# Kernel tuning notes

Measured on AMD Instinct MI355X. Metric: run time of the kernel, lower is better.

The kernel has to match this reference:

```python
import jax, jax.numpy as jnp
import numpy as np

N_NODES = 100000
N_EDGES = 1600000
NEG_SLOPE = 0.2


def gat_conv(x, W, al, ar, src, dst, n_nodes):
    """DGL-style GATConv. x:[N,Fin] W:[Fin,H*D] al,ar:[H,D] -> [N,H,D]."""
    H, D = al.shape
    h = (x @ W).reshape(-1, H, D)                      # [N,H,D]
    el = jnp.sum(h * al, axis=-1)                      # [N,H]
    er = jnp.sum(h * ar, axis=-1)                      # [N,H]
    e = jax.nn.leaky_relu(el[src] + er[dst], NEG_SLOPE)  # [E,H]
    # segment softmax over edges grouped by destination node
    m = jax.ops.segment_max(e, dst, num_segments=n_nodes)  # [N,H]
    ex = jnp.exp(e - m[dst])                           # [E,H]
    s = jax.ops.segment_sum(ex, dst, num_segments=n_nodes)  # [N,H]
    alpha = ex / s[dst]                                # [E,H]
    msg = h[src] * alpha[..., None]                    # [E,H,D]
    return jax.ops.segment_sum(msg, dst, num_segments=n_nodes)  # [N,H,D]


def setup_inputs() -> dict:
    key = jax.random.key(0)
    ks = jax.random.split(key, 9)
    in_dim, hid, out_dim, heads = 128, 32, 64, 4
    x = jax.random.normal(ks[0], (N_NODES, in_dim), dtype=jnp.float32)
    src = jax.random.randint(ks[1], (N_EDGES,), 0, N_NODES, dtype=jnp.int32)
    dst = jax.random.randint(ks[2], (N_EDGES,), 0, N_NODES, dtype=jnp.int32)
    sc1 = 1.0 / np.sqrt(in_dim)
    sc2 = 1.0 / np.sqrt(heads * hid)
    W1 = jax.random.normal(ks[3], (in_dim, heads * hid), dtype=jnp.float32) * sc1
    al1 = jax.random.normal(ks[4], (heads, hid), dtype=jnp.float32) * sc1
    ar1 = jax.random.normal(ks[5], (heads, hid), dtype=jnp.float32) * sc1
    W2 = jax.random.normal(ks[6], (heads * hid, out_dim), dtype=jnp.float32) * sc2
    al2 = jax.random.normal(ks[7], (1, out_dim), dtype=jnp.float32) * sc2
    ar2 = jax.random.normal(ks[8], (1, out_dim), dtype=jnp.float32) * sc2
    return {"x": x, "src": src, "dst": dst, "W1": W1, "al1": al1, "ar1": ar1,
            "W2": W2, "al2": al2, "ar2": ar2}


def reference(x, src, dst, W1, al1, ar1, W2, al2, ar2):
    h = gat_conv(x, W1, al1, ar1, src, dst, N_NODES)   # [N,4,32]
    h = h.reshape(h.shape[0], -1)                      # flatten(1) -> [N,128]
    h = jax.nn.selu(h)                                 # dropout is identity in eval
    out = gat_conv(h, W2, al2, ar2, src, dst, N_NODES) # [N,1,64]
    return out.mean(axis=1)                            # [N,64]
```

## Files before the change

kernel.cpp:

```cpp
#include <hip/hip_runtime.h>
#include <hip/hip_fp16.h>

#define N_NODES 100000
#define N_EDGES 1600000
#define NP1 (N_NODES + 1)
#define NB 391
#define CHUNK 6250
#define NBLK 256

static __device__ __forceinline__ unsigned pkh2(float a, float b) {
    __half2 t = __floats2half2_rn(a, b);
    return *(unsigned*)&t;
}

static __device__ __forceinline__ void fmix2(float& a_lo, float& a_hi,
                                             unsigned hw, float a) {
    asm("v_fma_mix_f32 %0, %1, %2, %0 op_sel:[0,0,0] op_sel_hi:[1,0,0]"
        : "+v"(a_lo) : "v"(hw), "v"(a));
    asm("v_fma_mix_f32 %0, %1, %2, %0 op_sel:[1,0,0] op_sel_hi:[1,0,0]"
        : "+v"(a_hi) : "v"(hw), "v"(a));
}

static __device__ __forceinline__ void fmix8(float* acc, uint4 v, float a) {
    fmix2(acc[0], acc[1], v.x, a);
    fmix2(acc[2], acc[3], v.y, a);
    fmix2(acc[4], acc[5], v.z, a);
    fmix2(acc[6], acc[7], v.w, a);
}

__global__ __launch_bounds__(256) void k_gemm1(
    const float* __restrict__ x, const float* __restrict__ W,
    const float* __restrict__ al, const float* __restrict__ ar,
    __half* __restrict__ h, float* __restrict__ el, float* __restrict__ er)
{
    __shared__ float xT[32 * 132];
    __shared__ float Wl[32 * 132];
    const int tid = threadIdx.x;
    const int n0 = blockIdx.x * 128;
    const int tc = tid & 15, tr = tid >> 4;
    const int r0 = tr * 8, c0 = tc * 8;

    float acc[8][8];
    #pragma unroll
    for (int i = 0; i < 8; ++i)
        #pragma unroll
        for (int j = 0; j < 8; ++j) acc[i][j] = 0.f;

    for (int kb = 0; kb < 128; kb += 32) {
        {
            const int k4 = (tid & 7) * 4;
            const int rr = tid >> 3;
            #pragma unroll
            for (int ii = 0; ii < 4; ++ii) {
                int row = rr + ii * 32;
                int n = n0 + row;
                float4 v = make_float4(0.f, 0.f, 0.f, 0.f);
                if (n < N_NODES) v = *(const float4*)(x + (size_t)n * 128 + kb + k4);
                xT[(k4 + 0) * 132 + row] = v.x;
                xT[(k4 + 1) * 132 + row] = v.y;
                xT[(k4 + 2) * 132 + row] = v.z;
                xT[(k4 + 3) * 132 + row] = v.w;
            }
        }
        {
            const int c4 = (tid & 31) * 4;
            const int kr = tid >> 5;
            #pragma unroll
            for (int ii = 0; ii < 4; ++ii) {
                int kk = kr + ii * 8;
                float4 w = *(const float4*)(W + (size_t)(kb + kk) * 128 + c4);
                *(float4*)(Wl + kk * 132 + c4) = w;
            }
        }
        __syncthreads();
        #pragma unroll 4
        for (int k = 0; k < 32; ++k) {
            float4 a0 = *(const float4*)(xT + k * 132 + r0);
            float4 a1 = *(const float4*)(xT + k * 132 + r0 + 4);
            float4 b0 = *(const float4*)(Wl + k * 132 + c0);
            float4 b1 = *(const float4*)(Wl + k * 132 + c0 + 4);
            float a[8] = {a0.x, a0.y, a0.z, a0.w, a1.x, a1.y, a1.z, a1.w};
            float b[8] = {b0.x, b0.y, b0.z, b0.w, b1.x, b1.y, b1.z, b1.w};
            #pragma unroll
            for (int i = 0; i < 8; ++i)
                #pragma unroll
                for (int j = 0; j < 8; ++j) acc[i][j] = fmaf(a[i], b[j], acc[i][j]);
        }
        __syncthreads();
    }

    float alv[8], arv[8];
    #pragma unroll
    for (int j = 0; j < 8; ++j) { alv[j] = al[c0 + j]; arv[j] = ar[c0 + j]; }
    #pragma unroll
    for (int i = 0; i < 8; ++i) {
        int n = n0 + r0 + i;
        float pl = 0.f, pr = 0.f;
        #pragma unroll
        for (int j = 0; j < 8; ++j) {
            pl = fmaf(acc[i][j], alv[j], pl);
            pr = fmaf(acc[i][j], arv[j], pr);
        }
        pl += __shfl_xor(pl, 1); pl += __shfl_xor(pl, 2);
        pr += __shfl_xor(pr, 1); pr += __shfl_xor(pr, 2);
        if (n < N_NODES) {
            uint4 o;
            o.x = pkh2(acc[i][0], acc[i][1]);
            o.y = pkh2(acc[i][2], acc[i][3]);
            o.z = pkh2(acc[i][4], acc[i][5]);
            o.w = pkh2(acc[i][6], acc[i][7]);
            *(uint4*)(h + (size_t)n * 128 + c0) = o;
            if ((tc & 3) == 0) {
                el[n * 4 + (tc >> 2)] = pl;
                er[n * 4 + (tc >> 2)] = pr;
            }
        }
    }
}

__global__ __launch_bounds__(256) void k_gemm2(
    const __half* __restrict__ in, const float* __restrict__ W,
    const float* __restrict__ al, const float* __restrict__ ar,
    __half* __restrict__ h, float* __restrict__ el, float* __restrict__ er)
{
    __shared__ float xT[32 * 132];
    __shared__ float Wl[32 * 68];
    const int tid = threadIdx.x;
    const int n0 = blockIdx.x * 128;
    const int tc = tid & 7, tr = tid >> 3;
    const int r0 = tr * 4, c0 = tc * 8;
    const float SC = 1.0507009873554805f;
    const float AL = 1.6732632423543772f;

    float acc[4][8];
    #pragma unroll
    for (int i = 0; i < 4; ++i)
        #pragma unroll
        for (int j = 0; j < 8; ++j) acc[i][j] = 0.f;

    for (int kb = 0; kb < 128; kb += 32) {
        {
            const int k4 = (tid & 7) * 4;
            const int rr = tid >> 3;
            #pragma unroll
            for (int ii = 0; ii < 4; ++ii) {
                int row = rr + ii * 32;
                int n = n0 + row;
                float4 v = make_float4(0.f, 0.f, 0.f, 0.f);
                if (n < N_NODES) {
                    uint2 u = *(const uint2*)(in + (size_t)n * 128 + kb + k4);
                    float2 f01 = __half22float2(*(__half2*)&u.x);
                    float2 f23 = __half22float2(*(__half2*)&u.y);
                    v = make_float4(f01.x, f01.y, f23.x, f23.y);
                }
                v.x = v.x > 0.f ? SC * v.x : SC * AL * (__expf(v.x) - 1.f);
                v.y = v.y > 0.f ? SC * v.y : SC * AL * (__expf(v.y) - 1.f);
                v.z = v.z > 0.f ? SC * v.z : SC * AL * (__expf(v.z) - 1.f);
                v.w = v.w > 0.f ? SC * v.w : SC * AL * (__expf(v.w) - 1.f);
                xT[(k4 + 0) * 132 + row] = v.x;
                xT[(k4 + 1) * 132 + row] = v.y;
                xT[(k4 + 2) * 132 + row] = v.z;
                xT[(k4 + 3) * 132 + row] = v.w;
            }
        }
        {
            const int c4 = (tid & 15) * 4;
            const int kr = tid >> 4;
            #pragma unroll
            for (int ii = 0; ii < 2; ++ii) {
                int kk = kr + ii * 16;
                float4 w = *(const float4*)(W + (size_t)(kb + kk) * 64 + c4);
                *(float4*)(Wl + kk * 68 + c4) = w;
            }
        }
        __syncthreads();
        #pragma unroll 4
        for (int k = 0; k < 32; ++k) {
            float4 a0 = *(const float4*)(xT + k * 132 + r0);
            float4 b0 = *(const float4*)(Wl + k * 68 + c0);
            float4 b1 = *(const float4*)(Wl + k * 68 + c0 + 4);
            float a[4] = {a0.x, a0.y, a0.z, a0.w};
            float b[8] = {b0.x, b0.y, b0.z, b0.w, b1.x, b1.y, b1.z, b1.w};
            #pragma unroll
            for (int i = 0; i < 4; ++i)
                #pragma unroll
                for (int j = 0; j < 8; ++j) acc[i][j] = fmaf(a[i], b[j], acc[i][j]);
        }
        __syncthreads();
    }

    float alv[8], arv[8];
    #pragma unroll
    for (int j = 0; j < 8; ++j) { alv[j] = al[c0 + j]; arv[j] = ar[c0 + j]; }
    #pragma unroll
    for (int i = 0; i < 4; ++i) {
        int n = n0 + r0 + i;
        float pl = 0.f, pr = 0.f;
        #pragma unroll
        for (int j = 0; j < 8; ++j) {
            pl = fmaf(acc[i][j], alv[j], pl);
            pr = fmaf(acc[i][j], arv[j], pr);
        }
        pl += __shfl_xor(pl, 1); pl += __shfl_xor(pl, 2); pl += __shfl_xor(pl, 4);
        pr += __shfl_xor(pr, 1); pr += __shfl_xor(pr, 2); pr += __shfl_xor(pr, 4);
        if (n < N_NODES) {
            uint4 o;
            o.x = pkh2(acc[i][0], acc[i][1]);
            o.y = pkh2(acc[i][2], acc[i][3]);
            o.z = pkh2(acc[i][4], acc[i][5]);
            o.w = pkh2(acc[i][6], acc[i][7]);
            *(uint4*)(h + (size_t)n * 64 + c0) = o;
            if (tc == 0) { el[n] = pl; er[n] = pr; }
        }
    }
}

__global__ __launch_bounds__(256) void k_bhist_tot(
    const int* __restrict__ dst, int* __restrict__ btot)
{
    __shared__ int cnt[NB];
    const int tid = threadIdx.x;
    for (int j = tid; j < NB; j += 256) cnt[j] = 0;
    __syncthreads();
    int beg = blockIdx.x * CHUNK, end = beg + CHUNK;
    for (int i = beg + tid; i < end; i += 256)
        atomicAdd(&cnt[dst[i] >> 8], 1);
    __syncthreads();
    for (int j = tid; j < NB; j += 256)
        if (cnt[j]) atomicAdd(&btot[j], cnt[j]);
}

__global__ __launch_bounds__(512) void k_bscan(
    const int* __restrict__ btot, int* __restrict__ boffs, int* __restrict__ cursor)
{
    __shared__ int tmp[512];
    int t = threadIdx.x;
    int v = (t < NB) ? btot[t] : 0;
    tmp[t] = v;
    __syncthreads();
    for (int o = 1; o < 512; o <<= 1) {
        int u = (t >= o) ? tmp[t - o] : 0;
        __syncthreads();
        tmp[t] += u;
        __syncthreads();
    }
    if (t < NB) { boffs[t] = tmp[t] - v; cursor[t] = tmp[t] - v; }
    if (t == 0) boffs[NB] = N_EDGES;
}

__global__ __launch_bounds__(256) void k_place(
    const int* __restrict__ src, const int* __restrict__ dst,
    int* __restrict__ cursor, unsigned* __restrict__ pairs)
{
    __shared__ int cnt[NB], basev[NB];
    const int tid = threadIdx.x;
    for (int j = tid; j < NB; j += 256) cnt[j] = 0;
    __syncthreads();
    int beg = blockIdx.x * CHUNK, end = beg + CHUNK;
    for (int i = beg + tid; i < end; i += 256)
        atomicAdd(&cnt[dst[i] >> 8], 1);
    __syncthreads();
    for (int j = tid; j < NB; j += 256)
        basev[j] = cnt[j] ? atomicAdd(&cursor[j], cnt[j]) : 0;
    __syncthreads();
    for (int j = tid; j < NB; j += 256) cnt[j] = 0;
    __syncthreads();
    for (int i = beg + tid; i < end; i += 256) {
        int d = dst[i];
        int b = d >> 8;
        int r = atomicAdd(&cnt[b], 1);
        pairs[basev[b] + r] = ((unsigned)(d & 255) << 17) | (unsigned)src[i];
    }
}

__global__ __launch_bounds__(256) void k_csr(
    const unsigned* __restrict__ pairs, const int* __restrict__ boffs,
    int* __restrict__ rowptr, int* __restrict__ csr_src)
{
    __shared__ int cnt[256], exc[256];
    const int b = blockIdx.x;
    const int tid = threadIdx.x;
    cnt[tid] = 0;
    __syncthreads();
    int beg = boffs[b];
    int end = boffs[b + 1];
    for (int i = beg + tid; i < end; i += 256)
        atomicAdd(&cnt[pairs[i] >> 17], 1);
    __syncthreads();
    int v = cnt[tid];
    exc[tid] = v;
    __syncthreads();
    for (int o = 1; o < 256; o <<= 1) {
        int t = (tid >= o) ? exc[tid - o] : 0;
        __syncthreads();
        exc[tid] += t;
        __syncthreads();
    }
    int excl = exc[tid] - v;
    int node = b * 256 + tid;
    if (node <= N_NODES) rowptr[node] = beg + excl;
    __syncthreads();
    exc[tid] = beg + excl;
    cnt[tid] = 0;
    __syncthreads();
    for (int i = beg + tid; i < end; i += 256) {
        unsigned e = pairs[i];
        int dl = (int)(e >> 17);
        int r = atomicAdd(&cnt[dl], 1);
        csr_src[exc[dl] + r] = (int)(e & 0x1FFFFu);
    }
}

__global__ __launch_bounds__(256) void k_fused1(
    const int* __restrict__ rowptr, const int* __restrict__ csr_src,
    const __half* __restrict__ h,
    const float* __restrict__ el,
    const float* __restrict__ er,
    __half* __restrict__ out)
{
    __shared__ int   s_sx[4][64];
    __shared__ float s_p[4][64][4];
    const int w = threadIdx.x >> 6;
    int node = (blockIdx.x << 2) + w;
    int lane = threadIdx.x & 63;
    if (node >= N_NODES) return;
    int rs = rowptr[node], re = rowptr[node + 1];
    const int q = lane & 15, g = lane >> 4;
    const int hq = q >> 2;
    float4 erd = ((const float4*)er)[node];
    float m0, m1, m2, m3;
    float s0 = 0.f, s1 = 0.f, s2 = 0.f, s3 = 0.f;
    float acc[8];
    #pragma unroll
    for (int k = 0; k < 8; ++k) acc[k] = 0.f;

    auto agg = [&](int nch) {
        int nit4 = (nch + 15) >> 4;
        for (int t = 0; t < nit4; ++t) {
            int eb = t * 16 + g;
            int sj0 = s_sx[w][eb];
            int sj1 = s_sx[w][eb + 4];
            int sj2 = s_sx[w][eb + 8];
            int sj3 = s_sx[w][eb + 12];
            float a0 = s_p[w][eb][hq];
            float a1 = s_p[w][eb + 4][hq];
            float a2 = s_p[w][eb + 8][hq];
            float a3 = s_p[w][eb + 12][hq];
            uint4 v0 = *((const uint4*)(h + (size_t)sj0 * 128) + q);
            uint4 v1 = *((const uint4*)(h + (size_t)sj1 * 128) + q);
            uint4 v2 = *((const uint4*)(h + (size_t)sj2 * 128) + q);
            uint4 v3 = *((const uint4*)(h + (size_t)sj3 * 128) + q);
            fmix8(acc, v0, a0);
            fmix8(acc, v1, a1);
            fmix8(acc, v2, a2);
            fmix8(acc, v3, a3);
        }
    };

    if (re > rs) {
        int nch = min(64, re - rs);
        int sidx = 0;
        float e0 = -INFINITY, e1 = -INFINITY, e2 = -INFINITY, e3 = -INFINITY;
        if (lane < nch) {
            sidx = csr_src[rs + lane];
            float4 l4 = ((const float4*)el)[sidx];
            e0 = l4.x + erd.x; e0 = e0 >= 0.f ? e0 : 0.2f * e0;
            e1 = l4.y + erd.y; e1 = e1 >= 0.f ? e1 : 0.2f * e1;
            e2 = l4.z + erd.z; e2 = e2 >= 0.f ? e2 : 0.2f * e2;
            e3 = l4.w + erd.w; e3 = e3 >= 0.f ? e3 : 0.2f * e3;
        }
        float c0 = e0, c1 = e1, c2 = e2, c3 = e3;
        #pragma unroll
        for (int o = 32; o > 0; o >>= 1) {
            c0 = fmaxf(c0, __shfl_xor(c0, o));
            c1 = fmaxf(c1, __shfl_xor(c1, o));
            c2 = fmaxf(c2, __shfl_xor(c2, o));
            c3 = fmaxf(c3, __shfl_xor(c3, o));
        }
        m0 = c0; m1 = c1; m2 = c2; m3 = c3;
        float p0 = __expf(e0 - m0), p1 = __expf(e1 - m1);
        float p2 = __expf(e2 - m2), p3 = __expf(e3 - m3);
        s_sx[w][lane] = sidx;
        *(float4*)&s_p[w][lane][0] = make_float4(p0, p1, p2, p3);
        float q0 = p0, q1 = p1, q2 = p2, q3 = p3;
        #pragma unroll
        for (int o = 32; o > 0; o >>= 1) {
            q0 += __shfl_xor(q0, o);
            q1 += __shfl_xor(q1, o);
            q2 += __shfl_xor(q2, o);
            q3 += __shfl_xor(q3, o);
        }
        s0 = q0; s1 = q1; s2 = q2; s3 = q3;
        agg(nch);

        for (int base = rs + 64; base < re; base += 64) {
            nch = min(64, re - base);
            sidx = 0;
            e0 = e1 = e2 = e3 = -INFINITY;
            if (lane < nch) {
                sidx = csr_src[base + lane];
                float4 l4 = ((const float4*)el)[sidx];
                e0 = l4.x + erd.x; e0 = e0 >= 0.f ? e0 : 0.2f * e0;
                e1 = l4.y + erd.y; e1 = e1 >= 0.f ? e1 : 0.2f * e1;
                e2 = l4.z + erd.z; e2 = e2 >= 0.f ? e2 : 0.2f * e2;
                e3 = l4.w + erd.w; e3 = e3 >= 0.f ? e3 : 0.2f * e3;
            }
            c0 = e0; c1 = e1; c2 = e2; c3 = e3;
            #pragma unroll
            for (int o = 32; o > 0; o >>= 1) {
                c0 = fmaxf(c0, __shfl_xor(c0, o));
                c1 = fmaxf(c1, __shfl_xor(c1, o));
                c2 = fmaxf(c2, __shfl_xor(c2, o));
                c3 = fmaxf(c3, __shfl_xor(c3, o));
            }
            float n0 = fmaxf(m0, c0), n1 = fmaxf(m1, c1);
            float n2 = fmaxf(m2, c2), n3 = fmaxf(m3, c3);
            float r0 = __expf(m0 - n0), r1 = __expf(m1 - n1);
            float r2 = __expf(m2 - n2), r3 = __expf(m3 - n3);
            p0 = __expf(e0 - n0); p1 = __expf(e1 - n1);
            p2 = __expf(e2 - n2); p3 = __expf(e3 - n3);
            s_sx[w][lane] = sidx;
            *(float4*)&s_p[w][lane][0] = make_float4(p0, p1, p2, p3);
            q0 = p0; q1 = p1; q2 = p2; q3 = p3;
            #pragma unroll
            for (int o = 32; o > 0; o >>= 1) {
                q0 += __shfl_xor(q0, o);
                q1 += __shfl_xor(q1, o);
                q2 += __shfl_xor(q2, o);
                q3 += __shfl_xor(q3, o);
            }
            s0 = s0 * r0 + q0; s1 = s1 * r1 + q1;
            s2 = s2 * r2 + q2; s3 = s3 * r3 + q3;
            float rh = hq == 0 ? r0 : hq == 1 ? r1 : hq == 2 ? r2 : r3;
            #pragma unroll
            for (int k = 0; k < 8; ++k) acc[k] *= rh;
            m0 = n0; m1 = n1; m2 = n2; m3 = n3;
            agg(nch);
        }
    }

    float sh = hq == 0 ? s0 : hq == 1 ? s1 : hq == 2 ? s2 : s3;
    float inv = (re > rs) ? 1.f / sh : 0.f;
    #pragma unroll
    for (int k = 0; k < 8; ++k) {
        acc[k] *= inv;
        acc[k] += __shfl_xor(acc[k], 16);
        acc[k] += __shfl_xor(acc[k], 32);
    }
    if (g == 0) {
        uint4 o;
        o.x = pkh2(acc[0], acc[1]);
        o.y = pkh2(acc[2], acc[3]);
        o.z = pkh2(acc[4], acc[5]);
        o.w = pkh2(acc[6], acc[7]);
        *((uint4*)(out + (size_t)node * 128) + q) = o;
    }
}

__global__ __launch_bounds__(256) void k_fused2(
    const int* __restrict__ rowptr, const int* __restrict__ csr_src,
    const __half* __restrict__ h,
    const float* __restrict__ el,
    const float* __restrict__ er,
    float* __restrict__ out)
{
    __shared__ int   s_sx[4][64];
    __shared__ float s_p[4][64];
    const int w = threadIdx.x >> 6;
    int node = (blockIdx.x << 2) + w;
    int lane = threadIdx.x & 63;
    if (node >= N_NODES) return;
    int rs = rowptr[node], re = rowptr[node + 1];
    const int q = lane & 7, g = lane >> 3;
    float erd = er[node];
    float m, s = 0.f;
    float acc[8];
    #pragma unroll
    for (int k = 0; k < 8; ++k) acc[k] = 0.f;

    auto agg = [&](int nch) {
        int nit4 = (nch + 31) >> 5;
        for (int t = 0; t < nit4; ++t) {
            int eb = t * 32 + g;
            int sj0 = s_sx[w][eb];
            int sj1 = s_sx[w][eb + 8];
            int sj2 = s_sx[w][eb + 16];
            int sj3 = s_sx[w][eb + 24];
            float a0 = s_p[w][eb];
            float a1 = s_p[w][eb + 8];
            float a2 = s_p[w][eb + 16];
            float a3 = s_p[w][eb + 24];
            uint4 v0 = *((const uint4*)(h + (size_t)sj0 * 64) + q);
            uint4 v1 = *((const uint4*)(h + (size_t)sj1 * 64) + q);
            uint4 v2 = *((const uint4*)(h + (size_t)sj2 * 64) + q);
            uint4 v3 = *((const uint4*)(h + (size_t)sj3 * 64) + q);
            fmix8(acc, v0, a0);
            fmix8(acc, v1, a1);
            fmix8(acc, v2, a2);
            fmix8(acc, v3, a3);
        }
    };

    if (re > rs) {
        int nch = min(64, re - rs);
        int sidx = 0;
        float e = -INFINITY;
        if (lane < nch) {
            sidx = csr_src[rs + lane];
            e = el[sidx] + erd;
            e = e >= 0.f ? e : 0.2f * e;
        }
        float c = e;
        #pragma unroll
        for (int o = 32; o > 0; o >>= 1) c = fmaxf(c, __shfl_xor(c, o));
        m = c;
        float p = __expf(e - m);
        s_sx[w][lane] = sidx;
        s_p[w][lane] = p;
        float qq = p;
        #pragma unroll
        for (int o = 32; o > 0; o >>= 1) qq += __shfl_xor(qq, o);
        s = qq;
        agg(nch);

        for (int base = rs + 64; base < re; base += 64) {
            nch = min(64, re - base);
            sidx = 0;
            e = -INFINITY;
            if (lane < nch) {
                sidx = csr_src[base + lane];
                e = el[sidx] + erd;
                e = e >= 0.f ? e : 0.2f * e;
            }
            c = e;
            #pragma unroll
            for (int o = 32; o > 0; o >>= 1) c = fmaxf(c, __shfl_xor(c, o));
            float n = fmaxf(m, c);
            float r = __expf(m - n);
            p = __expf(e - n);
            s_sx[w][lane] = sidx;
            s_p[w][lane] = p;
            float qq2 = p;
            #pragma unroll
            for (int o = 32; o > 0; o >>= 1) qq2 += __shfl_xor(qq2, o);
            s = s * r + qq2;
            #pragma unroll
            for (int k = 0; k < 8; ++k) acc[k] *= r;
            m = n;
            agg(nch);
        }
    }

    float inv = (re > rs) ? 1.f / s : 0.f;
    #pragma unroll
    for (int k = 0; k < 8; ++k) {
        acc[k] *= inv;
        acc[k] += __shfl_xor(acc[k], 8);
        acc[k] += __shfl_xor(acc[k], 16);
        acc[k] += __shfl_xor(acc[k], 32);
    }
    if (g == 0) {
        float* op = out + (size_t)node * 64 + q * 8;
        *(float4*)(op)     = make_float4(acc[0], acc[1], acc[2], acc[3]);
        *(float4*)(op + 4) = make_float4(acc[4], acc[5], acc[6], acc[7]);
    }
}

extern "C" void kernel_launch(void* const* d_in, const int* in_sizes, int n_in,
                              void* d_out, int out_size, void* d_ws, size_t ws_size,
                              hipStream_t stream) {
    const float* x   = (const float*)d_in[0];
    const int*   src = (const int*)d_in[1];
    const int*   dst = (const int*)d_in[2];
    const float* W1  = (const float*)d_in[3];
    const float* al1 = (const float*)d_in[4];
    const float* ar1 = (const float*)d_in[5];
    const float* W2  = (const float*)d_in[6];
    const float* al2 = (const float*)d_in[7];
    const float* ar2 = (const float*)d_in[8];
    float* out = (float*)d_out;

    char* base = (char*)d_ws;
    __half* h1   = (__half*)base;   base += (size_t)N_NODES * 128 * 2;
    __half* out1 = (__half*)base;   base += (size_t)N_NODES * 128 * 2;
    float*  el1  = (float*)base;    base += (size_t)N_NODES * 4 * 4;
    float*  er1  = (float*)base;    base += (size_t)N_NODES * 4 * 4;
    int* rowptr  = (int*)base;      base += (size_t)100004 * 4;
    int* btot    = (int*)base;      base += 512 * 4;
    int* boffs   = (int*)base;      base += 512 * 4;
    int* cursor  = (int*)base;      base += 512 * 4;
    int* csr_src = (int*)base;      base += (size_t)N_EDGES * 4;
    unsigned* pairs = (unsigned*)base; base += (size_t)N_EDGES * 4;
    __half* h2   = h1;
    float*  el2  = (float*)((char*)h1 + (size_t)N_NODES * 64 * 2);
    float*  er2  = el2 + N_NODES;

    const int GB = (N_NODES + 127) / 128;

    hipMemsetAsync(btot, 0, NB * sizeof(int), stream);
    k_bhist_tot<<<NBLK, 256, 0, stream>>>(dst, btot);
    k_bscan<<<1, 512, 0, stream>>>(btot, boffs, cursor);
    k_place<<<NBLK, 256, 0, stream>>>(src, dst, cursor, pairs);
    k_csr<<<NB, 256, 0, stream>>>(pairs, boffs, rowptr, csr_src);

    k_gemm1<<<GB, 256, 0, stream>>>(x, W1, al1, ar1, h1, el1, er1);
    k_fused1<<<(N_NODES + 3) / 4, 256, 0, stream>>>(rowptr, csr_src, h1, el1, er1, out1);

    k_gemm2<<<GB, 256, 0, stream>>>(out1, W2, al2, ar2, h2, el2, er2);
    k_fused2<<<(N_NODES + 3) / 4, 256, 0, stream>>>(rowptr, csr_src, h2, el2, er2, out);
}
```

Before: 272.6 us.

## Use fp16 MFMA matrix cores for both GAT projection GEMMs

Both dense projection kernels move from FP32 register-tiled FMA loops to fp16 MFMA 16x16x32 instructions. Inputs and weights are converted to half and staged in shared memory, with weights transposed. Outputs are staged back through shared memory so global stores are coalesced, and the tile shrinks to 64 nodes per block. This cuts GEMM compute time, but the fp16 inputs and weights lower precision, and the GEMMs are likely a small share of total time next to the edge aggregation kernels.

After: 252.0 us. -7.6%, faster.

```diff
diff --git a/kernel.cpp b/kernel.cpp
--- a/kernel.cpp
+++ b/kernel.cpp
@@ -8,6 +8,9 @@
 #define CHUNK 6250
 #define NBLK 256
 
+typedef _Float16 half8 __attribute__((ext_vector_type(8)));
+typedef float f32x4 __attribute__((ext_vector_type(4)));
+
 static __device__ __forceinline__ unsigned pkh2(float a, float b) {
     __half2 t = __floats2half2_rn(a, b);
     return *(unsigned*)&t;
@@ -33,87 +36,115 @@
     const float* __restrict__ al, const float* __restrict__ ar,
     __half* __restrict__ h, float* __restrict__ el, float* __restrict__ er)
 {
-    __shared__ float xT[32 * 132];
-    __shared__ float Wl[32 * 132];
+    __shared__ _Float16 Wt[128 * 136];
+    __shared__ _Float16 xs[64 * 136];
     const int tid = threadIdx.x;
-    const int n0 = blockIdx.x * 128;
-    const int tc = tid & 15, tr = tid >> 4;
-    const int r0 = tr * 8, c0 = tc * 8;
-
-    float acc[8][8];
-    #pragma unroll
-    for (int i = 0; i < 8; ++i)
-        #pragma unroll
-        for (int j = 0; j < 8; ++j) acc[i][j] = 0.f;
-
-    for (int kb = 0; kb < 128; kb += 32) {
-        {
-            const int k4 = (tid & 7) * 4;
-            const int rr = tid >> 3;
-            #pragma unroll
-            for (int ii = 0; ii < 4; ++ii) {
-                int row = rr + ii * 32;
-                int n = n0 + row;
-                float4 v = make_float4(0.f, 0.f, 0.f, 0.f);
-                if (n < N_NODES) v = *(const float4*)(x + (size_t)n * 128 + kb + k4);
-                xT[(k4 + 0) * 132 + row] = v.x;
-                xT[(k4 + 1) * 132 + row] = v.y;
-                xT[(k4 + 2) * 132 + row] = v.z;
-                xT[(k4 + 3) * 132 + row] = v.w;
+    const int n0 = blockIdx.x * 64;
+
+    #pragma unroll
+    for (int pass = 0; pass < 16; ++pass) {
+        int k  = (tid >> 5) + pass * 8;
+        int c4 = (tid & 31) * 4;
+        float4 w = *(const float4*)(W + (size_t)k * 128 + c4);
+        Wt[(c4 + 0) * 136 + k] = (_Float16)w.x;
+        Wt[(c4 + 1) * 136 + k] = (_Float16)w.y;
+        Wt[(c4 + 2) * 136 + k] = (_Float16)w.z;
+        Wt[(c4 + 3) * 136 + k] = (_Float16)w.w;
+    }
+    {
+        int row = tid >> 2, kq = (tid & 3) * 32;
+        int n = n0 + row;
+        _Float16* d = xs + row * 136 + kq;
+        if (n < N_NODES) {
+            const float* xp = x + (size_t)n * 128 + kq;
+            #pragma unroll
+            for (int j = 0; j < 8; ++j) {
+                float4 v = *(const float4*)(xp + j * 4);
+                d[j*4+0] = (_Float16)v.x; d[j*4+1] = (_Float16)v.y;
+                d[j*4+2] = (_Float16)v.z; d[j*4+3] = (_Float16)v.w;
             }
-        }
-        {
-            const int c4 = (tid & 31) * 4;
-            const int kr = tid >> 5;
-            #pragma unroll
-            for (int ii = 0; ii < 4; ++ii) {
-                int kk = kr + ii * 8;
-                float4 w = *(const float4*)(W + (size_t)(kb + kk) * 128 + c4);
-                *(float4*)(Wl + kk * 132 + c4) = w;
+        } else {
+            #pragma unroll
+            for (int j = 0; j < 32; ++j) d[j] = (_Float16)0.f;
+        }
+    }
+    __syncthreads();
+
+    const int wv = tid >> 6, l = tid & 63;
+    const int r0 = wv * 16;
+    const int lc = l & 15, lk = l >> 4;
+
+    half8 afr[4];
+    #pragma unroll
+    for (int ks = 0; ks < 4; ++ks)
+        afr[ks] = *(const half8*)(xs + (r0 + lc) * 136 + ks * 32 + lk * 8);
+    __syncthreads();
+
+    float eh_l[4][4], eh_r[4][4];
+    #pragma unroll
+    for (int hd = 0; hd < 4; ++hd)
+        #pragma unroll
+        for (int i = 0; i < 4; ++i) { eh_l[hd][i] = 0.f; eh_r[hd][i] = 0.f; }
+
+    f32x4 accs[8];
+    #pragma unroll
+    for (int ct = 0; ct < 8; ++ct) {
+        f32x4 acc = {0.f, 0.f, 0.f, 0.f};
+        #pragma unroll
+        for (int ks = 0; ks < 4; ++ks) {
+            half8 b = *(const half8*)(Wt + (ct * 16 + lc) * 136 + ks * 32 + lk * 8);
+            acc = __builtin_amdgcn_mfma_f32_16x16x32_f16(afr[ks], b, acc, 0, 0, 0);
+        }
+        accs[ct] = acc;
+        float a_l = al[ct * 16 + lc], a_r = ar[ct * 16 + lc];
+        #pragma unroll
+        for (int i = 0; i < 4; ++i) {
+            eh_l[ct >> 1][i] = fmaf(acc[i], a_l, eh_l[ct >> 1][i]);
+            eh_r[ct >> 1][i] = fmaf(acc[i], a_r, eh_r[ct >> 1][i]);
+        }
+    }
+
+    #pragma unroll
+    for (int ct = 0; ct < 8; ++ct)
+        #pragma unroll
+        for (int i = 0; i < 4; ++i)
+            xs[(r0 + lk * 4 + i) * 136 + ct * 16 + lc] = (_Float16)accs[ct][i];
+
+    #pragma unroll
+    for (int hd = 0; hd < 4; ++hd)
+        #pragma unroll
+        for (int i = 0; i < 4; ++i) {
+            float v = eh_l[hd][i];
+            v += __shfl_xor(v, 1); v += __shfl_xor(v, 2);
+            v += __shfl_xor(v, 4); v += __shfl_xor(v, 8);
+            eh_l[hd][i] = v;
+            float u = eh_r[hd][i];
+            u += __shfl_xor(u, 1); u += __shfl_xor(u, 2);
+            u += __shfl_xor(u, 4); u += __shfl_xor(u, 8);
+            eh_r[hd][i] = u;
+        }
+    if (lc == 0) {
+        #pragma unroll
+        for (int i = 0; i < 4; ++i) {
+            int n = n0 + r0 + lk * 4 + i;
+            if (n < N_NODES) {
+                #pragma unroll
+                for (int hd = 0; hd < 4; ++hd) {
+                    el[n * 4 + hd] = eh_l[hd][i];
+                    er[n * 4 + hd] = eh_r[hd][i];
+                }
             }
         }
-        __syncthreads();
-        #pragma unroll 4
-        for (int k = 0; k < 32; ++k) {
-            float4 a0 = *(const float4*)(xT + k * 132 + r0);
-            float4 a1 = *(const float4*)(xT + k * 132 + r0 + 4);
-            float4 b0 = *(const float4*)(Wl + k * 132 + c0);
-            float4 b1 = *(const float4*)(Wl + k * 132 + c0 + 4);
-            float a[8] = {a0.x, a0.y, a0.z, a0.w, a1.x, a1.y, a1.z, a1.w};
-            float b[8] = {b0.x, b0.y, b0.z, b0.w, b1.x, b1.y, b1.z, b1.w};
-            #pragma unroll
-            for (int i = 0; i < 8; ++i)
-                #pragma unroll
-                for (int j = 0; j < 8; ++j) acc[i][j] = fmaf(a[i], b[j], acc[i][j]);
-        }
-        __syncthreads();
-    }
-
-    float alv[8], arv[8];
-    #pragma unroll
-    for (int j = 0; j < 8; ++j) { alv[j] = al[c0 + j]; arv[j] = ar[c0 + j]; }
-    #pragma unroll
-    for (int i = 0; i < 8; ++i) {
-        int n = n0 + r0 + i;
-        float pl = 0.f, pr = 0.f;
-        #pragma unroll
-        for (int j = 0; j < 8; ++j) {
-            pl = fmaf(acc[i][j], alv[j], pl);
-            pr = fmaf(acc[i][j], arv[j], pr);
-        }
-        pl += __shfl_xor(pl, 1); pl += __shfl_xor(pl, 2);
-        pr += __shfl_xor(pr, 1); pr += __shfl_xor(pr, 2);
+    }
+    __syncthreads();
+    {
+        int row = tid >> 2, kq = (tid & 3) * 32;
+        int n = n0 + row;
         if (n < N_NODES) {
-            uint4 o;
-            o.x = pkh2(acc[i][0], acc[i][1]);
-            o.y = pkh2(acc[i][2], acc[i][3]);
-            o.z = pkh2(acc[i][4], acc[i][5]);
-            o.w = pkh2(acc[i][6], acc[i][7]);
-            *(uint4*)(h + (size_t)n * 128 + c0) = o;
-            if ((tc & 3) == 0) {
-                el[n * 4 + (tc >> 2)] = pl;
-                er[n * 4 + (tc >> 2)] = pr;
-            }
+            #pragma unroll
+            for (int j = 0; j < 4; ++j)
+                *(uint4*)(h + (size_t)n * 128 + kq + j * 8) =
+                    *(const uint4*)(xs + row * 136 + kq + j * 8);
         }
     }
 }
@@ -123,94 +154,113 @@
     const float* __restrict__ al, const float* __restrict__ ar,
     __half* __restrict__ h, float* __restrict__ el, float* __restrict__ er)
 {
-    __shared__ float xT[32 * 132];
-    __shared__ float Wl[32 * 68];
+    __shared__ _Float16 Wt[64 * 136];
+    __shared__ _Float16 xs[64 * 136];
     const int tid = threadIdx.x;
-    const int n0 = blockIdx.x * 128;
-    const int tc = tid & 7, tr = tid >> 3;
-    const int r0 = tr * 4, c0 = tc * 8;
+    const int n0 = blockIdx.x * 64;
     const float SC = 1.0507009873554805f;
     const float AL = 1.6732632423543772f;
 
-    float acc[4][8];
-    #pragma unroll
-    for (int i = 0; i < 4; ++i)
-        #pragma unroll
-        for (int j = 0; j < 8; ++j) acc[i][j] = 0.f;
-
-    for (int kb = 0; kb < 128; kb += 32) {
-        {
-            const int k4 = (tid & 7) * 4;
-            const int rr = tid >> 3;
-            #pragma unroll
-            for (int ii = 0; ii < 4; ++ii) {
-                int row = rr + ii * 32;
-                int n = n0 + row;
-                float4 v = make_float4(0.f, 0.f, 0.f, 0.f);
-                if (n < N_NODES) {
-                    uint2 u = *(const uint2*)(in + (size_t)n * 128 + kb + k4);
-                    float2 f01 = __half22float2(*(__half2*)&u.x);
-                    float2 f23 = __half22float2(*(__half2*)&u.y);
-                    v = make_float4(f01.x, f01.y, f23.x, f23.y);
-                }
-                v.x = v.x > 0.f ? SC * v.x : SC * AL * (__expf(v.x) - 1.f);
-                v.y = v.y > 0.f ? SC * v.y : SC * AL * (__expf(v.y) - 1.f);
-                v.z = v.z > 0.f ? SC * v.z : SC * AL * (__expf(v.z) - 1.f);
-                v.w = v.w > 0.f ? SC * v.w : SC * AL * (__expf(v.w) - 1.f);
-                xT[(k4 + 0) * 132 + row] = v.x;
-                xT[(k4 + 1) * 132 + row] = v.y;
-                xT[(k4 + 2) * 132 + row] = v.z;
-                xT[(k4 + 3) * 132 + row] = v.w;
+    #pragma unroll
+    for (int pass = 0; pass < 8; ++pass) {
+        int k  = (tid >> 4) + pass * 16;
+        int c4 = (tid & 15) * 4;
+        float4 w = *(const float4*)(W + (size_t)k * 64 + c4);
+        Wt[(c4 + 0) * 136 + k] = (_Float16)w.x;
+        Wt[(c4 + 1) * 136 + k] = (_Float16)w.y;
+        Wt[(c4 + 2) * 136 + k] = (_Float16)w.z;
+        Wt[(c4 + 3) * 136 + k] = (_Float16)w.w;
+    }
+    {
+        int row = tid >> 2, kq = (tid & 3) * 32;
+        int n = n0 + row;
+        _Float16* d = xs + row * 136 + kq;
+        if (n < N_NODES) {
+            const __half* ip = in + (size_t)n * 128 + kq;
+            #pragma unroll
+            for (int j = 0; j < 8; ++j) {
+                uint2 u = *(const uint2*)(ip + j * 4);
+                float2 f01 = __half22float2(*(__half2*)&u.x);
+                float2 f23 = __half22float2(*(__half2*)&u.y);
+                float v0 = f01.x > 0.f ? SC * f01.x : SC * AL * (__expf(f01.x) - 1.f);
+                float v1 = f01.y > 0.f ? SC * f01.y : SC * AL * (__expf(f01.y) - 1.f);
+                float v2 = f23.x > 0.f ? SC * f23.x : SC * AL * (__expf(f23.x) - 1.f);
+                float v3 = f23.y > 0.f ? SC * f23.y : SC * AL * (__expf(f23.y) - 1.f);
+                d[j*4+0] = (_Float16)v0; d[j*4+1] = (_Float16)v1;
+                d[j*4+2] = (_Float16)v2; d[j*4+3] = (_Float16)v3;
             }
-        }
-        {
-            const int c4 = (tid & 15) * 4;
-            const int kr = tid >> 4;
-            #pragma unroll
-            for (int ii = 0; ii < 2; ++ii) {
-                int kk = kr + ii * 16;
-                float4 w = *(const float4*)(W + (size_t)(kb + kk) * 64 + c4);
-                *(float4*)(Wl + kk * 68 + c4) = w;
-            }
-        }
-        __syncthreads();
-        #pragma unroll 4
-        for (int k = 0; k < 32; ++k) {
-            float4 a0 = *(const float4*)(xT + k * 132 + r0);
-            float4 b0 = *(const float4*)(Wl + k * 68 + c0);
-            float4 b1 = *(const float4*)(Wl + k * 68 + c0 + 4);
-            float a[4] = {a0.x, a0.y, a0.z, a0.w};
-            float b[8] = {b0.x, b0.y, b0.z, b0.w, b1.x, b1.y, b1.z, b1.w};
-            #pragma unroll
-            for (int i = 0; i < 4; ++i)
-                #pragma unroll
-                for (int j = 0; j < 8; ++j) acc[i][j] = fmaf(a[i], b[j], acc[i][j]);
-        }
-        __syncthreads();
-    }
-
-    float alv[8], arv[8];
-    #pragma unroll
-    for (int j = 0; j < 8; ++j) { alv[j] = al[c0 + j]; arv[j] = ar[c0 + j]; }
+        } else {
+            #pragma unroll
+            for (int j = 0; j < 32; ++j) d[j] = (_Float16)0.f;
+        }
+    }
+    __syncthreads();
+
+    const int wv = tid >> 6, l = tid & 63;
+    const int r0 = wv * 16;
+    const int lc = l & 15, lk = l >> 4;
+
+    half8 afr[4];
+    #pragma unroll
+    for (int ks = 0; ks < 4; ++ks)
+        afr[ks] = *(const half8*)(xs + (r0 + lc) * 136 + ks * 32 + lk * 8);
+    __syncthreads();
+
+    float pl[4], pr[4];
+    #pragma unroll
+    for (int i = 0; i < 4; ++i) { pl[i] = 0.f; pr[i] = 0.f; }
+
+    f32x4 accs[4];
+    #pragma unroll
+    for (int ct = 0; ct < 4; ++ct) {
+        f32x4 acc = {0.f, 0.f, 0.f, 0.f};
+        #pragma unroll
+        for (int ks = 0; ks < 4; ++ks) {
+            half8 b = *(const half8*)(Wt + (ct * 16 + lc) * 136 + ks * 32 + lk * 8);
+            acc = __builtin_amdgcn_mfma_f32_16x16x32_f16(afr[ks], b, acc, 0, 0, 0);
+        }
+        accs[ct] = acc;
+        float a_l = al[ct * 16 + lc], a_r = ar[ct * 16 + lc];
+        #pragma unroll
+        for (int i = 0; i < 4; ++i) {
+            pl[i] = fmaf(acc[i], a_l, pl[i]);
+            pr[i] = fmaf(acc[i], a_r, pr[i]);
+        }
+    }
+
+    #pragma unroll
+    for (int ct = 0; ct < 4; ++ct)
+        #pragma unroll
+        for (int i = 0; i < 4; ++i)
+            xs[(r0 + lk * 4 + i) * 136 + ct * 16 + lc] = (_Float16)accs[ct][i];
+
     #pragma unroll
     for (int i = 0; i < 4; ++i) {
-        int n = n0 + r0 + i;
-        float pl = 0.f, pr = 0.f;
-        #pragma unroll
-        for (int j = 0; j < 8; ++j) {
-            pl = fmaf(acc[i][j], alv[j], pl);
-            pr = fmaf(acc[i][j], arv[j], pr);
-        }
-        pl += __shfl_xor(pl, 1); pl += __shfl_xor(pl, 2); pl += __shfl_xor(pl, 4);
-        pr += __shfl_xor(pr, 1); pr += __shfl_xor(pr, 2); pr += __shfl_xor(pr, 4);
+        float v = pl[i];
+        v += __shfl_xor(v, 1); v += __shfl_xor(v, 2);
+        v += __shfl_xor(v, 4); v += __shfl_xor(v, 8);
+        pl[i] = v;
+        float u = pr[i];
+        u += __shfl_xor(u, 1); u += __shfl_xor(u, 2);
+        u += __shfl_xor(u, 4); u += __shfl_xor(u, 8);
+        pr[i] = u;
+    }
+    if (lc == 0) {
+        #pragma unroll
+        for (int i = 0; i < 4; ++i) {
+            int n = n0 + r0 + lk * 4 + i;
+            if (n < N_NODES) { el[n] = pl[i]; er[n] = pr[i]; }
+        }
+    }
+    __syncthreads();
+    {
+        int row = tid >> 2, kq = (tid & 3) * 16;
+        int n = n0 + row;
         if (n < N_NODES) {
-            uint4 o;
-            o.x = pkh2(acc[i][0], acc[i][1]);
-            o.y = pkh2(acc[i][2], acc[i][3]);
-            o.z = pkh2(acc[i][4], acc[i][5]);
-            o.w = pkh2(acc[i][6], acc[i][7]);
-            *(uint4*)(h + (size_t)n * 64 + c0) = o;
-            if (tc == 0) { el[n] = pl; er[n] = pr; }
+            #pragma unroll
+            for (int j = 0; j < 2; ++j)
+                *(uint4*)(h + (size_t)n * 64 + kq + j * 8) =
+                    *(const uint4*)(xs + row * 136 + kq + j * 8);
         }
     }
 }
@@ -595,7 +645,7 @@
     float*  el2  = (float*)((char*)h1 + (size_t)N_NODES * 64 * 2);
     float*  er2  = el2 + N_NODES;
 
-    const int GB = (N_NODES + 127) / 128;
+    const int GB = (N_NODES + 63) / 64;
 
     hipMemsetAsync(btot, 0, NB * sizeof(int), stream);
     k_bhist_tot<<<NBLK, 256, 0, stream>>>(dst, btot);
```
